# Kernel tuning notes

Hardware: AMD Instinct MI355X
Metric: run time of the kernel (lower is better)

The kernel has to match this reference:

```python
import jax, jax.numpy as jnp
import numpy as np

B, N, C_IN, C_OUT, K, D_EMB = 64, 2048, 64, 64, 3, 10

def setup_inputs() -> dict:
    key = jax.random.key(0)
    k1, k2, k3, k4 = jax.random.split(key, 4)
    x = jax.random.normal(k1, (B, N, C_IN), dtype=jnp.float32)
    node_embeddings = jax.random.normal(k2, (N, D_EMB), dtype=jnp.float32)
    weights_pool = jax.random.normal(k3, (D_EMB, K, C_IN, C_OUT), dtype=jnp.float32) * 0.1
    bias_pool = jax.random.normal(k4, (D_EMB, C_OUT), dtype=jnp.float32) * 0.1
    return {"x": x, "node_embeddings": node_embeddings,
            "weights_pool": weights_pool, "bias_pool": bias_pool, "cheb_k": K}

def reference(x, node_embeddings, weights_pool, bias_pool, cheb_k):
    n = node_embeddings.shape[0]
    # adaptive adjacency: softmax over rows of relu(E E^T)
    supports = jax.nn.softmax(jax.nn.relu(node_embeddings @ node_embeddings.T), axis=1)  # [N,N]
    support_set = [jnp.eye(n, dtype=x.dtype), supports]
    for _ in range(2, cheb_k):
        support_set.append(2.0 * supports @ support_set[-1] - support_set[-2])
    supports_k = jnp.stack(support_set, axis=0)                     # [K,N,N]
    # per-node weights/bias generated from embedding
    weights = jnp.einsum('nd,dkio->nkio', node_embeddings, weights_pool)  # [N,K,Ci,Co]
    bias = node_embeddings @ bias_pool                               # [N,Co]
    # graph conv: gather Chebyshev-filtered features then per-node grouped GEMM
    x_g = jnp.einsum('knm,bmc->bnkc', supports_k, x)                 # [B,N,K,Ci]
    out = jnp.einsum('bnki,nkio->bno', x_g, weights) + bias          # [B,N,Co]
    return out
```

## Files before the change

### kernel.cpp

```cpp
#include <hip/hip_runtime.h>

typedef __attribute__((ext_vector_type(8))) short short8;
typedef __attribute__((ext_vector_type(4))) float f32x4;
typedef __attribute__((ext_vector_type(4))) unsigned short us4;
typedef __attribute__((ext_vector_type(8))) unsigned short us8;

constexpr int Bb = 64, Nn = 2048, CI = 64, CO = 64, KK = 3, DE = 10;
constexpr int NW = Bb * CI;
constexpr int WPSZ = KK * CI * CO;

__device__ __forceinline__ unsigned short f2bf(float f) {
  unsigned u = __float_as_uint(f);
  u += 0x7fff + ((u >> 16) & 1);
  return (unsigned short)(u >> 16);
}
__device__ __forceinline__ float bf2f(unsigned short h) {
  return __uint_as_float(((unsigned)h) << 16);
}
__device__ __forceinline__ void gl2lds16(const void* g, void* l) {
  __builtin_amdgcn_global_load_lds(
      (const __attribute__((address_space(1))) void*)g,
      (__attribute__((address_space(3))) void*)l, 16, 0, 0);
}

__global__ __launch_bounds__(256) void prep_kernel(
    const float* __restrict__ E, unsigned short* __restrict__ S,
    const float* __restrict__ x, unsigned short* __restrict__ Xrow,
    unsigned short* __restrict__ XT) {
  __shared__ float sh[64 * 65];
  const int bid = blockIdx.x, t = threadIdx.x;

  if (bid < 2048) {
    const int n = bid;
    float emb[DE];
#pragma unroll
    for (int d = 0; d < DE; d++) emb[d] = E[n * DE + d];
    float v[8], lmax = -1e30f;
#pragma unroll
    for (int j = 0; j < 8; j++) {
      const int m = t + j * 256;
      float dot = 0.f;
#pragma unroll
      for (int d = 0; d < DE; d++) dot += emb[d] * E[m * DE + d];
      v[j] = fmaxf(dot, 0.f);
      lmax = fmaxf(lmax, v[j]);
    }
    sh[t] = lmax;
    __syncthreads();
    for (int s = 128; s > 0; s >>= 1) {
      if (t < s) sh[t] = fmaxf(sh[t], sh[t + s]);
      __syncthreads();
    }
    const float rowmax = sh[0];
    __syncthreads();
    float lsum = 0.f;
#pragma unroll
    for (int j = 0; j < 8; j++) { v[j] = __expf(v[j] - rowmax); lsum += v[j]; }
    sh[t] = lsum;
    __syncthreads();
    for (int s = 128; s > 0; s >>= 1) {
      if (t < s) sh[t] += sh[t + s];
      __syncthreads();
    }
    const float inv = 1.f / sh[0];
#pragma unroll
    for (int j = 0; j < 8; j++) S[(size_t)n * Nn + t + j * 256] = f2bf(v[j] * inv);
  } else {
    const int id = bid - 2048;
    const int b = id & 63, n0 = (id >> 6) * 64;
    const int i4 = (t & 15) * 4;
#pragma unroll
    for (int j = 0; j < 4; j++) {
      const int r = j * 16 + (t >> 4);
      const float4 v =
          *(const float4*)(x + (size_t)b * (Nn * CI) + (size_t)(n0 + r) * CI + i4);
      us4 o; o.x = f2bf(v.x); o.y = f2bf(v.y); o.z = f2bf(v.z); o.w = f2bf(v.w);
      *(us4*)(Xrow + (size_t)(n0 + r) * NW + b * CI + i4) = o;
      sh[r * 65 + i4 + 0] = v.x; sh[r * 65 + i4 + 1] = v.y;
      sh[r * 65 + i4 + 2] = v.z; sh[r * 65 + i4 + 3] = v.w;
    }
    __syncthreads();
    const int i = t >> 2, c0 = (t & 3) * 16;
    us8 p0, p1;
#pragma unroll
    for (int j = 0; j < 8; j++) p0[j] = f2bf(sh[(c0 + j) * 65 + i]);
#pragma unroll
    for (int j = 0; j < 8; j++) p1[j] = f2bf(sh[(c0 + 8 + j) * 65 + i]);
    unsigned short* dst = XT + (size_t)(b * CI + i) * Nn + n0 + c0;
    *(us8*)(dst) = p0;
    *(us8*)(dst + 8) = p1;
  }
}

__global__ __launch_bounds__(256) void mfma_gemm(
    const unsigned short* __restrict__ A, const unsigned short* __restrict__ Bt,
    const unsigned short* __restrict__ Xsub, unsigned short* __restrict__ Crow,
    unsigned short* __restrict__ Ct, int mode) {
  __shared__ unsigned short sm[16384];
  unsigned short* As = sm;
  unsigned short* Bs = sm + 8192;
  const int t = threadIdx.x, lane = t & 63, wave = t >> 6;
  const int n0 = blockIdx.x * 128, m0 = blockIdx.y * 128;
  const int wm = (wave & 1) * 64, wn = (wave >> 1) * 64;
  const int lr = lane & 15, lq = lane >> 4;

  f32x4 acc[4][4] = {};
  const int srow = lane >> 3;
  const int schunk = (lane & 7) ^ srow;

  for (int k0 = 0; k0 < 2048; k0 += 64) {
    __syncthreads();
#pragma unroll
    for (int j = 0; j < 4; j++) {
      const int r0 = (wave * 4 + j) * 8;
      gl2lds16(A  + (size_t)(m0 + r0 + srow) * 2048 + k0 + schunk * 8, As + r0 * 64);
      gl2lds16(Bt + (size_t)(n0 + r0 + srow) * 2048 + k0 + schunk * 8, Bs + r0 * 64);
    }
    __syncthreads();
#pragma unroll
    for (int ks = 0; ks < 2; ks++) {
      short8 af[4], bfr[4];
#pragma unroll
      for (int i = 0; i < 4; i++) {
        const int m = wm + i * 16 + lr;
        const int slot = (ks * 4 + lq) ^ (m & 7);
        af[i] = *(const short8*)(As + m * 64 + slot * 8);
      }
#pragma unroll
      for (int j = 0; j < 4; j++) {
        const int n = wn + j * 16 + lr;
        const int slot = (ks * 4 + lq) ^ (n & 7);
        bfr[j] = *(const short8*)(Bs + n * 64 + slot * 8);
      }
#pragma unroll
      for (int i = 0; i < 4; i++)
#pragma unroll
        for (int j = 0; j < 4; j++)
          acc[i][j] = __builtin_amdgcn_mfma_f32_16x16x32_bf16(af[i], bfr[j], acc[i][j], 0, 0, 0);
    }
  }

  __syncthreads();
#pragma unroll
  for (int i = 0; i < 4; i++) {
#pragma unroll
    for (int r = 0; r < 4; r++) {
      const int m = wm + i * 16 + lq * 4 + r;
      const int sw = (m & 7) ^ ((m >> 3) & 7);
#pragma unroll
      for (int j = 0; j < 4; j++) {
        const int n = wn + j * 16 + lr;
        sm[m * 128 + (((n >> 3) ^ sw) * 8) + (n & 7)] = f2bf(acc[i][j][r]);
      }
    }
  }
  __syncthreads();

  {
    const int rr = t >> 4, cc = (t & 15) * 8;
#pragma unroll
    for (int p = 0; p < 8; p++) {
      const int m = p * 16 + rr;
      const int slot = (cc >> 3) ^ (m & 7) ^ ((m >> 3) & 7);
      us8 v = *(const us8*)(sm + m * 128 + slot * 8);
      if (mode == 1) {
        const us8 xv = *(const us8*)(Xsub + (size_t)(m0 + m) * NW + n0 + cc);
#pragma unroll
        for (int q = 0; q < 8; q++) v[q] = f2bf(2.f * bf2f(v[q]) - bf2f(xv[q]));
      }
      *(us8*)(Crow + (size_t)(m0 + m) * NW + n0 + cc) = v;
    }
  }
  if (mode == 0) {
    const int w = t >> 4, mc = (t & 15) * 8;
#pragma unroll
    for (int p = 0; p < 8; p++) {
      const int n = p * 16 + w;
      us8 v;
#pragma unroll
      for (int q = 0; q < 8; q++) {
        const int m = mc + q;
        v[q] = sm[m * 128 + (((n >> 3) ^ (m & 7) ^ ((m >> 3) & 7)) * 8) + (n & 7)];
      }
      *(us8*)(Ct + (size_t)(n0 + n) * 2048 + m0 + mc) = v;
    }
  }
}

__global__ __launch_bounds__(256) void wgen_kernel(
    const float* __restrict__ E, const float* __restrict__ Wp,
    const float* __restrict__ bp, unsigned short* __restrict__ W_all,
    float* __restrict__ bias_all) {
  __shared__ float El[8 * DE];
  __shared__ float Wtl[5][1088];
  const int t = threadIdx.x;
  const int c = blockIdx.x >> 8;
  const int n0 = (blockIdx.x & 255) * 8;

  if (t < 8 * DE) El[t] = E[n0 * DE + t];
  __syncthreads();

  if (c == 0) {
#pragma unroll
    for (int j = 0; j < 2; j++) {
      const int idx = j * 256 + t;
      const int nl = idx >> 6, o = idx & 63;
      float b = 0.f;
#pragma unroll
      for (int d = 0; d < DE; d++) b += El[nl * DE + d] * bp[d * CO + o];
      bias_all[(size_t)(n0 + nl) * CO + o] = b;
    }
  }

  const int il = t >> 4, o4 = t & 15;
  const int oc = t >> 2, iq = t & 3;

  for (int p = 0; p < 4; p++) {
    float acc[8][4];
#pragma unroll
    for (int n = 0; n < 8; n++)
#pragma unroll
      for (int q = 0; q < 4; q++) acc[n][q] = 0.f;

#pragma unroll
    for (int h = 0; h < 2; h++) {
      __syncthreads();
#pragma unroll
      for (int j = 0; j < 5; j++) {
        const float4 w = *(const float4*)(Wp + (size_t)(h * 5 + j) * WPSZ +
                                          c * (CI * CO) + (p * 16 + il) * CO + o4 * 4);
        Wtl[j][(o4 * 4 + 0) * 17 + il] = w.x;
        Wtl[j][(o4 * 4 + 1) * 17 + il] = w.y;
        Wtl[j][(o4 * 4 + 2) * 17 + il] = w.z;
        Wtl[j][(o4 * 4 + 3) * 17 + il] = w.w;
      }
      __syncthreads();
      float wl[5][4];
#pragma unroll
      for (int d = 0; d < 5; d++)
#pragma unroll
        for (int q = 0; q < 4; q++) wl[d][q] = Wtl[d][oc * 17 + iq * 4 + q];
#pragma unroll
      for (int n = 0; n < 8; n++) {
#pragma unroll
        for (int d = 0; d < 5; d++) {
          const float e = El[n * DE + h * 5 + d];
#pragma unroll
          for (int q = 0; q < 4; q++) acc[n][q] += e * wl[d][q];
        }
      }
    }
#pragma unroll
    for (int n = 0; n < 8; n++) {
      us4 v;
#pragma unroll
      for (int q = 0; q < 4; q++) v[q] = f2bf(acc[n][q]);
      *(us4*)(W_all + (size_t)(n0 + n) * WPSZ + c * (CI * CO) +
              oc * 64 + p * 16 + iq * 4) = v;
    }
  }
}

__global__ __launch_bounds__(256) void out_kernel(
    const unsigned short* __restrict__ Xrow, const unsigned short* __restrict__ XG1,
    const unsigned short* __restrict__ XG2, const unsigned short* __restrict__ W_all,
    const float* __restrict__ bias_all, float* __restrict__ out) {
  __shared__ unsigned short Wt[KK * CO * 64];
  __shared__ unsigned short Al[KK * Bb * CI];

  const int n = blockIdx.x, t = threadIdx.x, lane = t & 63, wave = t >> 6;
  const unsigned short* srcs[KK] = {Xrow + (size_t)n * NW, XG1 + (size_t)n * NW,
                                    XG2 + (size_t)n * NW};
  const unsigned short* wsrc = W_all + (size_t)n * WPSZ;
  const int srow = lane >> 3;
  const int schunk = (lane & 7) ^ srow;
#pragma unroll
  for (int j = 0; j < 6; j++) {
    const int r0 = (wave * 6 + j) * 8;
    const int c = r0 >> 6, b0 = r0 & 63;
    gl2lds16(srcs[c] + (b0 + srow) * 64 + schunk * 8, Al + r0 * 64);
    gl2lds16(wsrc + (r0 + srow) * 64 + schunk * 8, Wt + r0 * 64);
  }

  const int lr = lane & 15, lq = lane >> 4;
  const float bias_o = bias_all[(size_t)n * CO + wave * 16 + lr];
  __syncthreads();

  f32x4 acc[4] = {};
#pragma unroll
  for (int kt = 0; kt < 6; kt++) {
    const int c = kt >> 1;
    const int chunk = (kt & 1) * 4 + lq;
    const int o = wave * 16 + lr;
    const short8 bfrag =
        *(const short8*)(Wt + (c * 64 + o) * 64 + (chunk ^ (o & 7)) * 8);
#pragma unroll
    for (int mt = 0; mt < 4; mt++) {
      const int b = mt * 16 + lr;
      const short8 afrag =
          *(const short8*)(Al + (c * 64 + b) * 64 + (chunk ^ (b & 7)) * 8);
      acc[mt] = __builtin_amdgcn_mfma_f32_16x16x32_bf16(afrag, bfrag, acc[mt], 0, 0, 0);
    }
  }

#pragma unroll
  for (int mt = 0; mt < 4; mt++) {
#pragma unroll
    for (int r = 0; r < 4; r++) {
      const int b = mt * 16 + lq * 4 + r;
      out[(size_t)b * (Nn * CO) + (size_t)n * CO + wave * 16 + lr] =
          acc[mt][r] + bias_o;
    }
  }
}

extern "C" void kernel_launch(void* const* d_in, const int* in_sizes, int n_in,
                              void* d_out, int out_size, void* d_ws,
                              size_t ws_size, hipStream_t stream) {
  const float* x  = (const float*)d_in[0];
  const float* E  = (const float*)d_in[1];
  const float* Wp = (const float*)d_in[2];
  const float* bp = (const float*)d_in[3];
  float* out = (float*)d_out;

  unsigned short* ws   = (unsigned short*)d_ws;
  unsigned short* Xrow = ws;
  unsigned short* XG1r = Xrow + (size_t)Nn * NW;
  unsigned short* XG2r = XG1r + (size_t)Nn * NW;
  unsigned short* S    = XG2r + (size_t)Nn * NW;
  unsigned short* XT   = S    + (size_t)Nn * Nn;
  unsigned short* XG1T = XT   + (size_t)NW * Nn;
  unsigned short* W_all = S;
  float* bias_all = (float*)(W_all + (size_t)Nn * WPSZ);

  prep_kernel<<<4096, 256, 0, stream>>>(E, S, x, Xrow, XT);

  dim3 g(NW / 128, Nn / 128);
  mfma_gemm<<<g, 256, 0, stream>>>(S, XT,   nullptr, XG1r, XG1T, 0);
  mfma_gemm<<<g, 256, 0, stream>>>(S, XG1T, Xrow,    XG2r, nullptr, 1);

  wgen_kernel<<<768, 256, 0, stream>>>(E, Wp, bp, W_all, bias_all);
  out_kernel<<<Nn, 256, 0, stream>>>(Xrow, XG1r, XG2r, W_all, bias_all, out);
}
```

Measured before the change: 247.1 us.

## Fold Chebyshev recurrence into weight pool, fuse weight generation into output kernel

The 2*S*XG1 - X term is moved into the weights: the pool is pre-combined (W0-W2, W1, 2*W2) in prep, so the second GEMM only stores S*XG1 with no subtraction epilogue. The separate wgen kernel and its large per-node weight buffer are removed. Each out_kernel block now builds its own bf16 weights and bias from the embedding and the combined pool. The GEMM tile also shrinks from 128x128 to 128x64, doubling block count. This adds on-the-fly weight compute per node and an extra bf16 rounding of the combined pool.

```diff
diff --git a/kernel.cpp b/kernel.cpp
--- a/kernel.cpp
+++ b/kernel.cpp
@@ -26,7 +26,8 @@
 __global__ __launch_bounds__(256) void prep_kernel(
     const float* __restrict__ E, unsigned short* __restrict__ S,
     const float* __restrict__ x, unsigned short* __restrict__ Xrow,
-    unsigned short* __restrict__ XT) {
+    unsigned short* __restrict__ XT, const float* __restrict__ Wp,
+    unsigned short* __restrict__ Wpf) {
   __shared__ float sh[64 * 65];
   const int bid = blockIdx.x, t = threadIdx.x;
 
@@ -65,7 +66,7 @@
     const float inv = 1.f / sh[0];
 #pragma unroll
     for (int j = 0; j < 8; j++) S[(size_t)n * Nn + t + j * 256] = f2bf(v[j] * inv);
-  } else {
+  } else if (bid < 4096) {
     const int id = bid - 2048;
     const int b = id & 63, n0 = (id >> 6) * 64;
     const int i4 = (t & 15) * 4;
@@ -89,22 +90,35 @@
     unsigned short* dst = XT + (size_t)(b * CI + i) * Nn + n0 + c0;
     *(us8*)(dst) = p0;
     *(us8*)(dst + 8) = p1;
+  } else {
+    const int e4 = ((bid - 4096) * 256 + t) * 4;
+    const int d = e4 / WPSZ;
+    const int r = e4 - d * WPSZ;
+    const int c = r >> 12, io = r & 4095;
+    float4 v = *(const float4*)(Wp + (size_t)d * WPSZ + c * 4096 + io);
+    if (c == 0) {
+      const float4 w2 = *(const float4*)(Wp + (size_t)d * WPSZ + 2 * 4096 + io);
+      v.x -= w2.x; v.y -= w2.y; v.z -= w2.z; v.w -= w2.w;
+    } else if (c == 2) {
+      v.x *= 2.f; v.y *= 2.f; v.z *= 2.f; v.w *= 2.f;
+    }
+    us4 o; o.x = f2bf(v.x); o.y = f2bf(v.y); o.z = f2bf(v.z); o.w = f2bf(v.w);
+    *(us4*)(Wpf + e4) = o;
   }
 }
 
 __global__ __launch_bounds__(256) void mfma_gemm(
     const unsigned short* __restrict__ A, const unsigned short* __restrict__ Bt,
-    const unsigned short* __restrict__ Xsub, unsigned short* __restrict__ Crow,
-    unsigned short* __restrict__ Ct, int mode) {
-  __shared__ unsigned short sm[16384];
+    unsigned short* __restrict__ Crow, unsigned short* __restrict__ Ct, int mode) {
+  __shared__ unsigned short sm[12288];
   unsigned short* As = sm;
   unsigned short* Bs = sm + 8192;
   const int t = threadIdx.x, lane = t & 63, wave = t >> 6;
-  const int n0 = blockIdx.x * 128, m0 = blockIdx.y * 128;
-  const int wm = (wave & 1) * 64, wn = (wave >> 1) * 64;
+  const int n0 = blockIdx.x * 64, m0 = blockIdx.y * 128;
+  const int wm = (wave & 1) * 64, wn = (wave >> 1) * 32;
   const int lr = lane & 15, lq = lane >> 4;
 
-  f32x4 acc[4][4] = {};
+  f32x4 acc[4][2] = {};
   const int srow = lane >> 3;
   const int schunk = (lane & 7) ^ srow;
 
@@ -113,13 +127,17 @@
 #pragma unroll
     for (int j = 0; j < 4; j++) {
       const int r0 = (wave * 4 + j) * 8;
-      gl2lds16(A  + (size_t)(m0 + r0 + srow) * 2048 + k0 + schunk * 8, As + r0 * 64);
+      gl2lds16(A + (size_t)(m0 + r0 + srow) * 2048 + k0 + schunk * 8, As + r0 * 64);
+    }
+#pragma unroll
+    for (int j = 0; j < 2; j++) {
+      const int r0 = (wave * 2 + j) * 8;
       gl2lds16(Bt + (size_t)(n0 + r0 + srow) * 2048 + k0 + schunk * 8, Bs + r0 * 64);
     }
     __syncthreads();
 #pragma unroll
     for (int ks = 0; ks < 2; ks++) {
-      short8 af[4], bfr[4];
+      short8 af[4], bfr[2];
 #pragma unroll
       for (int i = 0; i < 4; i++) {
         const int m = wm + i * 16 + lr;
@@ -127,7 +145,7 @@
         af[i] = *(const short8*)(As + m * 64 + slot * 8);
       }
 #pragma unroll
-      for (int j = 0; j < 4; j++) {
+      for (int j = 0; j < 2; j++) {
         const int n = wn + j * 16 + lr;
         const int slot = (ks * 4 + lq) ^ (n & 7);
         bfr[j] = *(const short8*)(Bs + n * 64 + slot * 8);
@@ -135,7 +153,7 @@
 #pragma unroll
       for (int i = 0; i < 4; i++)
 #pragma unroll
-        for (int j = 0; j < 4; j++)
+        for (int j = 0; j < 2; j++)
           acc[i][j] = __builtin_amdgcn_mfma_f32_16x16x32_bf16(af[i], bfr[j], acc[i][j], 0, 0, 0);
     }
   }
@@ -148,130 +166,53 @@
       const int m = wm + i * 16 + lq * 4 + r;
       const int sw = (m & 7) ^ ((m >> 3) & 7);
 #pragma unroll
-      for (int j = 0; j < 4; j++) {
+      for (int j = 0; j < 2; j++) {
         const int n = wn + j * 16 + lr;
-        sm[m * 128 + (((n >> 3) ^ sw) * 8) + (n & 7)] = f2bf(acc[i][j][r]);
+        sm[m * 64 + (((n >> 3) ^ sw) * 8) + (n & 7)] = f2bf(acc[i][j][r]);
       }
     }
   }
   __syncthreads();
 
   {
-    const int rr = t >> 4, cc = (t & 15) * 8;
-#pragma unroll
-    for (int p = 0; p < 8; p++) {
-      const int m = p * 16 + rr;
+    const int rr = t >> 3, cc = (t & 7) * 8;
+#pragma unroll
+    for (int p = 0; p < 4; p++) {
+      const int m = p * 32 + rr;
       const int slot = (cc >> 3) ^ (m & 7) ^ ((m >> 3) & 7);
-      us8 v = *(const us8*)(sm + m * 128 + slot * 8);
-      if (mode == 1) {
-        const us8 xv = *(const us8*)(Xsub + (size_t)(m0 + m) * NW + n0 + cc);
-#pragma unroll
-        for (int q = 0; q < 8; q++) v[q] = f2bf(2.f * bf2f(v[q]) - bf2f(xv[q]));
-      }
+      const us8 v = *(const us8*)(sm + m * 64 + slot * 8);
       *(us8*)(Crow + (size_t)(m0 + m) * NW + n0 + cc) = v;
     }
   }
   if (mode == 0) {
-    const int w = t >> 4, mc = (t & 15) * 8;
-#pragma unroll
-    for (int p = 0; p < 8; p++) {
-      const int n = p * 16 + w;
+    const int mc = (t & 15) * 8;
+#pragma unroll
+    for (int p = 0; p < 4; p++) {
+      const int n = p * 16 + (t >> 4);
       us8 v;
 #pragma unroll
       for (int q = 0; q < 8; q++) {
         const int m = mc + q;
-        v[q] = sm[m * 128 + (((n >> 3) ^ (m & 7) ^ ((m >> 3) & 7)) * 8) + (n & 7)];
+        v[q] = sm[m * 64 + (((n >> 3) ^ (m & 7) ^ ((m >> 3) & 7)) * 8) + (n & 7)];
       }
       *(us8*)(Ct + (size_t)(n0 + n) * 2048 + m0 + mc) = v;
     }
   }
 }
 
-__global__ __launch_bounds__(256) void wgen_kernel(
-    const float* __restrict__ E, const float* __restrict__ Wp,
-    const float* __restrict__ bp, unsigned short* __restrict__ W_all,
-    float* __restrict__ bias_all) {
-  __shared__ float El[8 * DE];
-  __shared__ float Wtl[5][1088];
-  const int t = threadIdx.x;
-  const int c = blockIdx.x >> 8;
-  const int n0 = (blockIdx.x & 255) * 8;
-
-  if (t < 8 * DE) El[t] = E[n0 * DE + t];
-  __syncthreads();
-
-  if (c == 0) {
-#pragma unroll
-    for (int j = 0; j < 2; j++) {
-      const int idx = j * 256 + t;
-      const int nl = idx >> 6, o = idx & 63;
-      float b = 0.f;
-#pragma unroll
-      for (int d = 0; d < DE; d++) b += El[nl * DE + d] * bp[d * CO + o];
-      bias_all[(size_t)(n0 + nl) * CO + o] = b;
-    }
-  }
-
-  const int il = t >> 4, o4 = t & 15;
-  const int oc = t >> 2, iq = t & 3;
-
-  for (int p = 0; p < 4; p++) {
-    float acc[8][4];
-#pragma unroll
-    for (int n = 0; n < 8; n++)
-#pragma unroll
-      for (int q = 0; q < 4; q++) acc[n][q] = 0.f;
-
-#pragma unroll
-    for (int h = 0; h < 2; h++) {
-      __syncthreads();
-#pragma unroll
-      for (int j = 0; j < 5; j++) {
-        const float4 w = *(const float4*)(Wp + (size_t)(h * 5 + j) * WPSZ +
-                                          c * (CI * CO) + (p * 16 + il) * CO + o4 * 4);
-        Wtl[j][(o4 * 4 + 0) * 17 + il] = w.x;
-        Wtl[j][(o4 * 4 + 1) * 17 + il] = w.y;
-        Wtl[j][(o4 * 4 + 2) * 17 + il] = w.z;
-        Wtl[j][(o4 * 4 + 3) * 17 + il] = w.w;
-      }
-      __syncthreads();
-      float wl[5][4];
-#pragma unroll
-      for (int d = 0; d < 5; d++)
-#pragma unroll
-        for (int q = 0; q < 4; q++) wl[d][q] = Wtl[d][oc * 17 + iq * 4 + q];
-#pragma unroll
-      for (int n = 0; n < 8; n++) {
-#pragma unroll
-        for (int d = 0; d < 5; d++) {
-          const float e = El[n * DE + h * 5 + d];
-#pragma unroll
-          for (int q = 0; q < 4; q++) acc[n][q] += e * wl[d][q];
-        }
-      }
-    }
-#pragma unroll
-    for (int n = 0; n < 8; n++) {
-      us4 v;
-#pragma unroll
-      for (int q = 0; q < 4; q++) v[q] = f2bf(acc[n][q]);
-      *(us4*)(W_all + (size_t)(n0 + n) * WPSZ + c * (CI * CO) +
-              oc * 64 + p * 16 + iq * 4) = v;
-    }
-  }
-}
-
 __global__ __launch_bounds__(256) void out_kernel(
     const unsigned short* __restrict__ Xrow, const unsigned short* __restrict__ XG1,
-    const unsigned short* __restrict__ XG2, const unsigned short* __restrict__ W_all,
-    const float* __restrict__ bias_all, float* __restrict__ out) {
+    const unsigned short* __restrict__ Yr, const float* __restrict__ E,
+    const unsigned short* __restrict__ Wpf, const float* __restrict__ bp,
+    float* __restrict__ out) {
   __shared__ unsigned short Wt[KK * CO * 64];
   __shared__ unsigned short Al[KK * Bb * CI];
+  __shared__ float biasl[CO];
 
   const int n = blockIdx.x, t = threadIdx.x, lane = t & 63, wave = t >> 6;
+
   const unsigned short* srcs[KK] = {Xrow + (size_t)n * NW, XG1 + (size_t)n * NW,
-                                    XG2 + (size_t)n * NW};
-  const unsigned short* wsrc = W_all + (size_t)n * WPSZ;
+                                    Yr + (size_t)n * NW};
   const int srow = lane >> 3;
   const int schunk = (lane & 7) ^ srow;
 #pragma unroll
@@ -279,13 +220,41 @@
     const int r0 = (wave * 6 + j) * 8;
     const int c = r0 >> 6, b0 = r0 & 63;
     gl2lds16(srcs[c] + (b0 + srow) * 64 + schunk * 8, Al + r0 * 64);
-    gl2lds16(wsrc + (r0 + srow) * 64 + schunk * 8, Wt + r0 * 64);
-  }
+  }
+
+  float emb[DE];
+#pragma unroll
+  for (int d = 0; d < DE; d++) emb[d] = E[n * DE + d];
+
+  const int o8 = (t & 7) * 8;
+#pragma unroll
+  for (int j = 0; j < 6; j++) {
+    const int c = j >> 1;
+    const int i = (j & 1) * 32 + (t >> 3);
+    float w[8] = {};
+#pragma unroll
+    for (int d = 0; d < DE; d++) {
+      const us8 wp = *(const us8*)(Wpf + (size_t)d * WPSZ + c * 4096 + i * 64 + o8);
+#pragma unroll
+      for (int q = 0; q < 8; q++) w[q] += emb[d] * bf2f(wp[q]);
+    }
+    const int chunk = i >> 3, ilo = i & 7;
+#pragma unroll
+    for (int q = 0; q < 8; q++) {
+      const int o = o8 + q;
+      Wt[(c * 64 + o) * 64 + ((chunk ^ (o & 7)) * 8) + ilo] = f2bf(w[q]);
+    }
+  }
+  if (t < CO) {
+    float bsum = 0.f;
+#pragma unroll
+    for (int d = 0; d < DE; d++) bsum += emb[d] * bp[d * CO + t];
+    biasl[t] = bsum;
+  }
+  __syncthreads();
 
   const int lr = lane & 15, lq = lane >> 4;
-  const float bias_o = bias_all[(size_t)n * CO + wave * 16 + lr];
-  __syncthreads();
-
+  const float bias_o = biasl[wave * 16 + lr];
   f32x4 acc[4] = {};
 #pragma unroll
   for (int kt = 0; kt < 6; kt++) {
@@ -326,19 +295,17 @@
   unsigned short* ws   = (unsigned short*)d_ws;
   unsigned short* Xrow = ws;
   unsigned short* XG1r = Xrow + (size_t)Nn * NW;
-  unsigned short* XG2r = XG1r + (size_t)Nn * NW;
-  unsigned short* S    = XG2r + (size_t)Nn * NW;
+  unsigned short* Yr   = XG1r + (size_t)Nn * NW;
+  unsigned short* S    = Yr   + (size_t)Nn * NW;
   unsigned short* XT   = S    + (size_t)Nn * Nn;
   unsigned short* XG1T = XT   + (size_t)NW * Nn;
-  unsigned short* W_all = S;
-  float* bias_all = (float*)(W_all + (size_t)Nn * WPSZ);
-
-  prep_kernel<<<4096, 256, 0, stream>>>(E, S, x, Xrow, XT);
-
-  dim3 g(NW / 128, Nn / 128);
-  mfma_gemm<<<g, 256, 0, stream>>>(S, XT,   nullptr, XG1r, XG1T, 0);
-  mfma_gemm<<<g, 256, 0, stream>>>(S, XG1T, Xrow,    XG2r, nullptr, 1);
-
-  wgen_kernel<<<768, 256, 0, stream>>>(E, Wp, bp, W_all, bias_all);
-  out_kernel<<<Nn, 256, 0, stream>>>(Xrow, XG1r, XG2r, W_all, bias_all, out);
-}
+  unsigned short* Wpf  = XG1T + (size_t)NW * Nn;
+
+  prep_kernel<<<4216, 256, 0, stream>>>(E, S, x, Xrow, XT, Wp, Wpf);
+
+  dim3 g(NW / 64, Nn / 128);
+  mfma_gemm<<<g, 256, 0, stream>>>(S, XT,   XG1r, XG1T, 0);
+  mfma_gemm<<<g, 256, 0, stream>>>(S, XG1T, Yr,   nullptr, 1);
+
+  out_kernel<<<Nn, 256, 0, stream>>>(Xrow, XG1r, Yr, E, Wpf, bp, out);
+}
```

Measured after the change: 221.3 us. 10.4% less time.
